# Kernel optimization log

Measured on AMD Instinct MI355X. Metric: run time of the kernel, lower is better.

The kernel has to match this reference:

```python
import jax, jax.numpy as jnp
import numpy as np

TIME_STEP = 3  # init_kwargs time_step
D = 512       # input_dim
N = 1024      # node_num
B = 16        # batch


def setup_inputs() -> dict:
    key = jax.random.key(0)
    ks = jax.random.split(key, 16)
    x = jax.random.normal(ks[0], (B, N, D), dtype=jnp.float32)
    # adjacency in [0,1), scaled by 1/N so repeated propagation stays well-conditioned
    in_matrix = jax.random.uniform(ks[1], (N, N), dtype=jnp.float32) / N
    out_matrix = jax.random.uniform(ks[2], (N, N), dtype=jnp.float32) / N
    s = 0.02
    w3w = jax.random.normal(ks[3], (D, 2 * D), dtype=jnp.float32) * s
    b3w = jnp.zeros((D,), dtype=jnp.float32)
    w3u = jax.random.normal(ks[4], (D, D), dtype=jnp.float32) * s
    b3u = jnp.zeros((D,), dtype=jnp.float32)
    w4w = jax.random.normal(ks[5], (D, 2 * D), dtype=jnp.float32) * s
    b4w = jnp.zeros((D,), dtype=jnp.float32)
    w5w = jax.random.normal(ks[6], (D, 2 * D), dtype=jnp.float32) * s
    b5w = jnp.zeros((D,), dtype=jnp.float32)
    w5u = jax.random.normal(ks[7], (D, D), dtype=jnp.float32) * s
    b5u = jnp.zeros((D,), dtype=jnp.float32)
    return {"x": x, "in_matrix": in_matrix, "out_matrix": out_matrix,
            "w3w": w3w, "b3w": b3w, "w3u": w3u, "b3u": b3u,
            "w4w": w4w, "b4w": b4w, "w5w": w5w, "b5w": b5w,
            "w5u": w5u, "b5u": b5u}


def reference(x, in_matrix, out_matrix, w3w, b3w, w3u, b3u, w4w, b4w, w5w, b5w, w5u, b5u):
    # x: [B, N, D]; in/out_matrix: [N, N] (shared across batch, as in torch repeat)
    nodes = x
    for _ in range(TIME_STEP):
        a_in = jnp.einsum('mn,bnd->bmd', in_matrix, nodes)   # [B,N,D]
        a_out = jnp.einsum('mn,bnd->bmd', out_matrix, nodes)  # [B,N,D]
        av = jnp.concatenate([a_in, a_out], axis=-1)           # [B,N,2D]
        f = nodes
        u3 = jnp.einsum('bnd,ed->bne', f, w3u) + b3u           # shared eq3_u term
        zv = jax.nn.sigmoid(jnp.einsum('bnc,ec->bne', av, w3w) + b3w + u3)
        # NOTE: original code reuses fc_eq3_u inside rv (faithful reproduction)
        rv = jax.nn.sigmoid(jnp.einsum('bnc,ec->bne', av, w4w) + b4w + u3)
        hv = jnp.tanh(jnp.einsum('bnc,ec->bne', av, w5w) + b5w
                      + jnp.einsum('bnd,ed->bne', rv * f, w5u) + b5u)
        nodes = (1.0 - zv) * f + zv * hv  # dropout p=0 -> identity
    return (nodes, in_matrix)
```

## Files before the change

kernel.cpp:

```cpp
#include <hip/hip_runtime.h>
#include <cstdint>
#include <cstddef>


#define B_ 16
#define N_ 1024
#define D_ 512
#define S_ (B_ * N_)
#define TWO_D 1024

typedef __attribute__((ext_vector_type(8))) short short8;
typedef __attribute__((ext_vector_type(4))) short s16x4;
typedef __attribute__((ext_vector_type(4))) float f32x4;

#define EPI_AVU3 0
#define EPI_BIG  2
#define EPI_G4   3

__device__ __forceinline__ float bf2f(short u) {
  union { unsigned int i; float f; } v;
  v.i = ((unsigned int)(unsigned short)u) << 16;
  return v.f;
}
__device__ __forceinline__ short f2bf(float f) {
  union { float f; unsigned int i; } v;
  v.f = f;
  unsigned int x = v.i;
  unsigned int r = (x + 0x7fffu + ((x >> 16) & 1u)) >> 16;
  return (short)(unsigned short)r;
}
__device__ __forceinline__ float fast_sigmoid(float x) {
  return __builtin_amdgcn_rcpf(1.f + __expf(-x));
}
__device__ __forceinline__ float fast_tanh(float x) {
  const float t = __expf(-2.f * fabsf(x));
  const float th = (1.f - t) * __builtin_amdgcn_rcpf(1.f + t);
  return __builtin_copysignf(th, x);
}

__device__ __forceinline__ void gload16(const void* g, void* l) {
  __builtin_amdgcn_global_load_lds(
      (__attribute__((address_space(1))) void*)g,
      (__attribute__((address_space(3))) void*)l, 16, 0, 0);
}

template <int EPI>
__global__ __launch_bounds__(512, 4) void gemm_nt(
    const short* A, const short* A2, int lda,
    const short* Bw, const short* Bw2, const short* Bw3, int ldb, int Kin,
    const float* bias0, const float* bias1, const float* bias2,
    const short* u3, const short* fcur,
    const short* hvp, const short* zvp,
    short* out0, short* out1, short* out2,
    float* outf, int twoC) {
  __shared__ __align__(16) short lds_a[128 * 32];
  __shared__ __align__(16) short lds_b[128 * 32];

  const int tid = threadIdx.x;
  const int lane = tid & 63;
  const int wave = tid >> 6;
  const int wr = wave >> 2;
  const int wc = wave & 3;

  int bx = blockIdx.x, by = blockIdx.y, bz = blockIdx.z;
  if constexpr (EPI == EPI_AVU3) {
    const int total = gridDim.x * gridDim.y * gridDim.z;
    const int id = (bz * gridDim.y + by) * gridDim.x + bx;
    if ((total & 7) == 0) {
      const int a = id & 7, m = id >> 3;
      const int l = a * (total >> 3) + m;
      bx = l & 3;
      by = (l >> 2) & 7;
      bz = l >> 5;
    }
  } else {
    const int gx = gridDim.x, gy = gridDim.y;
    if ((gy & 7) == 0) {
      const int id = by * gx + bx;
      const int a = id & 7;
      const int m = id >> 3;
      const int per = gy >> 3;
      by = a * per + m / gx;
      bx = m % gx;
    }
  }

  int m0 = by * 128;
  const int n0 = bx * 128;
  int K = Kin;

  const short* Aeff = A;
  const short* Beff = Bw;
  int lda_e = lda, ldb_e = ldb;
  int nb0 = n0;
  bool isU3 = false;
  int b_ = 0, j_ = 0;
  if constexpr (EPI == EPI_AVU3) {
    if (bz < twoC) {
      b_ = bz >> 1;
      j_ = bz & 1;
      Aeff = j_ ? A2 : A;
      Beff = Bw + (size_t)b_ * ((size_t)D_ * N_);
      lda_e = N_; ldb_e = N_; K = N_;
    } else {
      isU3 = true;
      const int b = bz - twoC;
      Aeff = u3  + (size_t)b * N_ * D_;
      Beff = Bw3 ;
      lda_e = D_; ldb_e = D_; K = D_;
      b_ = b;
    }
  } else if constexpr (EPI == EPI_BIG) {
    if (n0 < 512) { Beff = Bw; nb0 = n0; }
    else if (n0 < 1024) { Beff = Bw2; nb0 = n0 - 512; }
    else { Beff = Bw3; nb0 = n0 - 1024; }
  }

  f32x4 acc[4][2];
#pragma unroll
  for (int i = 0; i < 4; i++)
#pragma unroll
    for (int j = 0; j < 2; j++) acc[i][j] = (f32x4){0.f, 0.f, 0.f, 0.f};

  const int ar = tid >> 2;
  const int sc = tid & 3;
  const int qg = (sc - (ar >> 1)) & 3;
  const int ac = qg * 8;
  char* la = (char*)lds_a + tid * 16;
  char* lb = (char*)lds_b + tid * 16;
  const short* ga0 = Aeff + (size_t)(m0 + ar) * lda_e + ac;
  const short* gb0 = Beff + (size_t)(nb0 + ar) * ldb_e + ac;

  const int lm = lane & 15;
  const int qq = lane >> 4;

  int offA[4], offB[2];
#pragma unroll
  for (int i = 0; i < 4; i++) {
    const int Ra = wr * 64 + i * 16 + lm;
    offA[i] = Ra * 64 + (((qq + (Ra >> 1)) & 3) << 4);
  }
#pragma unroll
  for (int j = 0; j < 2; j++) {
    const int Rb = wc * 32 + j * 16 + lm;
    offB[j] = Rb * 64 + (((qq + (Rb >> 1)) & 3) << 4);
  }

  for (int k0 = 0; k0 < K; k0 += 32) {
    __syncthreads();
    gload16(ga0 + k0, la);
    gload16(gb0 + k0, lb);
    __syncthreads();

    short8 af[4], bfr[2];
#pragma unroll
    for (int i = 0; i < 4; i++)
      af[i] = *(const short8*)((const char*)lds_a + offA[i]);
#pragma unroll
    for (int j = 0; j < 2; j++)
      bfr[j] = *(const short8*)((const char*)lds_b + offB[j]);
#pragma unroll
    for (int i = 0; i < 4; i++)
#pragma unroll
      for (int j = 0; j < 2; j++)
        acc[i][j] = __builtin_amdgcn_mfma_f32_16x16x32_bf16(
            af[i], bfr[j], acc[i][j], 0, 0, 0);
  }

  const int r0 = (lane >> 4) * 4;
#pragma unroll
  for (int i = 0; i < 4; i++) {
#pragma unroll
    for (int j = 0; j < 2; j++) {
#pragma unroll
      for (int r = 0; r < 4; r++) {
        const int grow = m0 + wr * 64 + i * 16 + r0 + r;
        const int gcol = n0 + wc * 32 + j * 16 + lm;
        const float v = acc[i][j][r];
        if constexpr (EPI == EPI_AVU3) {
          if (!isU3) {
            out0[((size_t)(b_ * N_ + grow)) * TWO_D + j_ * D_ + gcol] =
                f2bf(v);
          } else {
            out1[((size_t)(b_ * N_ + grow)) * D_ + gcol] =
                f2bf(v + bias0[gcol]);
          }
        } else if constexpr (EPI == EPI_BIG) {
          if (gcol < 512) {
            const size_t sidx = (size_t)grow * D_ + gcol;
            const float x = v + bias0[gcol] + bf2f(u3[sidx]);
            out0[sidx] = f2bf(fast_sigmoid(x));
          } else if (gcol < 1024) {
            const int e = gcol - 512;
            const size_t sidx = (size_t)grow * D_ + e;
            const float x = v + bias1[e] + bf2f(u3[sidx]);
            out1[sidx] = f2bf(fast_sigmoid(x) * bf2f(fcur[sidx]));
          } else {
            const int e = gcol - 1024;
            const size_t sidx = (size_t)grow * D_ + e;
            out2[sidx] = f2bf(v + bias2[e]);
          }
        } else {
          const size_t sidx = (size_t)grow * D_ + gcol;
          const float x = bf2f(hvp[sidx]) + v + bias0[gcol];
          const float hv = fast_tanh(x);
          const float z = bf2f(zvp[sidx]);
          const float f = bf2f(fcur[sidx]);
          const float res = (1.f - z) * f + z * hv;
          if (outf) outf[sidx] = res;
          else out0[sidx] = f2bf(res);
        }
      }
    }
  }
}

__global__ void transpose_bnd(const short* __restrict__ in,
                              short* __restrict__ out) {
  __shared__ short tile[32][33];
  const int b = blockIdx.z;
  const int n0 = blockIdx.y * 32;
  const int d0 = blockIdx.x * 32;
  const int tx = threadIdx.x, ty = threadIdx.y;
  const short* ip = in + (size_t)b * N_ * D_;
  short* op = out + (size_t)b * N_ * D_;
#pragma unroll
  for (int yy = ty; yy < 32; yy += 8)
    tile[yy][tx] = ip[(size_t)(n0 + yy) * D_ + d0 + tx];
  __syncthreads();
#pragma unroll
  for (int yy = ty; yy < 32; yy += 8)
    op[(size_t)(d0 + yy) * N_ + n0 + tx] = tile[tx][yy];
}

struct CvtJobs {
  const float* src[8];
  short* dst[8];
  int end4[8];
  int tot4;
};
__global__ void cvt_all(CvtJobs j) {
  for (int idx = blockIdx.x * 256 + threadIdx.x; idx < j.tot4;
       idx += gridDim.x * 256) {
    int k = 0, start = 0;
#pragma unroll
    for (int t = 0; t < 8; t++) {
      if (idx >= j.end4[t]) { k = t + 1; start = j.end4[t]; }
    }
    const int rel = idx - start;
    const f32x4 v = ((const f32x4*)j.src[k])[rel];
    s16x4 o;
#pragma unroll
    for (int r = 0; r < 4; r++) o[r] = f2bf(v[r]);
    ((s16x4*)j.dst[k])[rel] = o;
  }
}

extern "C" void kernel_launch(void* const* d_in, const int* in_sizes, int n_in,
                              void* d_out, int out_size, void* d_ws,
                              size_t ws_size, hipStream_t stream) {
  const float* x = (const float*)d_in[0];
  const float* inM = (const float*)d_in[1];
  const float* outM = (const float*)d_in[2];
  const float* w3w = (const float*)d_in[3];
  const float* b3w = (const float*)d_in[4];
  const float* w3u = (const float*)d_in[5];
  const float* b3u = (const float*)d_in[6];
  const float* w4w = (const float*)d_in[7];
  const float* b4w = (const float*)d_in[8];
  const float* w5w = (const float*)d_in[9];
  const float* b5w = (const float*)d_in[10];
  const float* w5u = (const float*)d_in[11];
  const float* b5u = (const float*)d_in[12];
  float* outF = (float*)d_out;

  char* ws = (char*)d_ws;
  size_t off = 0;
  auto alloc = [&](size_t elems) {
    short* p = (short*)(ws + off);
    off = (off + elems * 2 + 255) & ~(size_t)255;
    return p;
  };
  short* nodes = alloc((size_t)S_ * D_);
  short* inMb = alloc((size_t)N_ * N_);
  short* outMb = alloc((size_t)N_ * N_);
  short* w3wb = alloc((size_t)512 * 1024);
  short* w4wb = alloc((size_t)512 * 1024);
  short* w5wb = alloc((size_t)512 * 1024);
  short* w3ub = alloc((size_t)D_ * D_);
  short* w5ub = alloc((size_t)D_ * D_);
  const size_t fixed = off;

  int C = 1;
  for (int c = 16; c >= 1; c >>= 1) {
    const size_t need = fixed + (size_t)7 * c * N_ * D_ * 2 + 8 * 256;
    if (need <= ws_size) { C = c; break; }
  }
  short* T = alloc((size_t)C * D_ * N_);
  short* av = alloc((size_t)C * N_ * TWO_D);
  short* u3 = alloc((size_t)C * N_ * D_);
  short* zv = alloc((size_t)C * N_ * D_);
  short* rf = alloc((size_t)C * N_ * D_);
  short* hvp = alloc((size_t)C * N_ * D_);

  CvtJobs cj;
  const int xs4 = S_ * D_ / 4, nn4 = N_ * N_ / 4;
  const int dd4 = D_ * D_ / 4, wd4 = 512 * 1024 / 4;
  const float* srcs[8] = {x, inM, outM, w3w, w4w, w5w, w3u, w5u};
  short* dsts[8] = {nodes, inMb, outMb, w3wb, w4wb, w5wb, w3ub, w5ub};
  const int lens[8] = {xs4, nn4, nn4, wd4, wd4, wd4, dd4, dd4};
  int cum = 0;
  for (int i = 0; i < 8; i++) {
    cj.src[i] = srcs[i];
    cj.dst[i] = dsts[i];
    cum += lens[i];
    cj.end4[i] = cum;
  }
  cj.tot4 = cum;
  cvt_all<<<1536, 256, 0, stream>>>(cj);
  hipMemcpyAsync(outF + (size_t)S_ * D_, inM, (size_t)N_ * N_ * 4,
                 hipMemcpyDeviceToDevice, stream);

  const dim3 tb32(32, 8);
  const dim3 tg(D_ / 32, N_ / 32, C);
  const dim3 g_avu3(D_ / 128, N_ / 128, 3 * C);
  const dim3 g_d(D_ / 128, C * N_ / 128, 1);
  const dim3 g_big(1536 / 128, C * N_ / 128, 1);

  const int nchunks = B_ / C;
  for (int c = 0; c < nchunks; ++c) {
    short* nodes_c = nodes + (size_t)c * C * N_ * D_;
    float* outF_c = outF + (size_t)c * C * N_ * D_;
    for (int step = 0; step < 3; ++step) {
      transpose_bnd<<<tg, tb32, 0, stream>>>(nodes_c, T);
      gemm_nt<EPI_AVU3><<<g_avu3, 512, 0, stream>>>(
          inMb, outMb, N_, T, nullptr, w3ub, N_, N_, b3u, nullptr, nullptr,
          nodes_c, nullptr, nullptr, nullptr, av, u3, nullptr, nullptr,
          2 * C);
      gemm_nt<EPI_BIG><<<g_big, 512, 0, stream>>>(
          av, nullptr, TWO_D, w3wb, w4wb, w5wb, TWO_D, TWO_D, b3w, b4w, b5w,
          u3, nodes_c, nullptr, nullptr, zv, rf, hvp, nullptr, 0);
      float* outf = (step == 2) ? outF_c : nullptr;
      gemm_nt<EPI_G4><<<g_d, 512, 0, stream>>>(
          rf, nullptr, D_, w5ub, nullptr, nullptr, D_, D_, b5u, nullptr,
          nullptr, nullptr, nodes_c, hvp, zv, nodes_c, nullptr, nullptr,
          outf, 0);
    }
  }
}
```

Baseline: 668.0 us.

## Double-buffer LDS tiles in GEMM to overlap global loads with MFMA

Adds a second pair of LDS buffers for the A and B tiles and restructures the K loop to prefetch the next 32-wide K slice while MFMAs consume the current one. This halves the number of barriers per K step and is meant to hide global-to-LDS load latency behind compute. LDS usage doubles to 32 KB per block, which may cut occupancy at 4 blocks of 512 threads per CU. The loop also assumes K is a multiple of 64.

New measurement: 636.8 us, median of 2. 1.05x faster.

```diff
diff --git a/kernel.cpp b/kernel.cpp
--- a/kernel.cpp
+++ b/kernel.cpp
@@ -53,8 +53,10 @@
     const short* hvp, const short* zvp,
     short* out0, short* out1, short* out2,
     float* outf, int twoC) {
-  __shared__ __align__(16) short lds_a[128 * 32];
-  __shared__ __align__(16) short lds_b[128 * 32];
+  __shared__ __align__(16) short lds_a0[128 * 32];
+  __shared__ __align__(16) short lds_b0[128 * 32];
+  __shared__ __align__(16) short lds_a1[128 * 32];
+  __shared__ __align__(16) short lds_b1[128 * 32];
 
   const int tid = threadIdx.x;
   const int lane = tid & 63;
@@ -126,8 +128,10 @@
   const int sc = tid & 3;
   const int qg = (sc - (ar >> 1)) & 3;
   const int ac = qg * 8;
-  char* la = (char*)lds_a + tid * 16;
-  char* lb = (char*)lds_b + tid * 16;
+  char* la0p = (char*)lds_a0 + tid * 16;
+  char* lb0p = (char*)lds_b0 + tid * 16;
+  char* la1p = (char*)lds_a1 + tid * 16;
+  char* lb1p = (char*)lds_b1 + tid * 16;
   const short* ga0 = Aeff + (size_t)(m0 + ar) * lda_e + ac;
   const short* gb0 = Beff + (size_t)(nb0 + ar) * ldb_e + ac;
 
@@ -146,26 +150,37 @@
     offB[j] = Rb * 64 + (((qq + (Rb >> 1)) & 3) << 4);
   }
 
-  for (int k0 = 0; k0 < K; k0 += 32) {
+#define COMPUTE_TILE(LA, LB)                                                 \
+  do {                                                                       \
+    short8 af[4], bfr[2];                                                    \
+    _Pragma("unroll") for (int i = 0; i < 4; i++)                            \
+        af[i] = *(const short8*)((const char*)(LA) + offA[i]);               \
+    _Pragma("unroll") for (int j = 0; j < 2; j++)                            \
+        bfr[j] = *(const short8*)((const char*)(LB) + offB[j]);              \
+    _Pragma("unroll") for (int i = 0; i < 4; i++)                            \
+        _Pragma("unroll") for (int j = 0; j < 2; j++)                        \
+            acc[i][j] = __builtin_amdgcn_mfma_f32_16x16x32_bf16(             \
+                af[i], bfr[j], acc[i][j], 0, 0, 0);                          \
+  } while (0)
+
+  gload16(ga0, la0p);
+  gload16(gb0, lb0p);
+  __syncthreads();
+
+  for (int k0 = 0; k0 < K; k0 += 64) {
+    gload16(ga0 + k0 + 32, la1p);
+    gload16(gb0 + k0 + 32, lb1p);
+    COMPUTE_TILE(lds_a0, lds_b0);
     __syncthreads();
-    gload16(ga0 + k0, la);
-    gload16(gb0 + k0, lb);
+
+    if (k0 + 64 < K) {
+      gload16(ga0 + k0 + 64, la0p);
+      gload16(gb0 + k0 + 64, lb0p);
+    }
+    COMPUTE_TILE(lds_a1, lds_b1);
     __syncthreads();
-
-    short8 af[4], bfr[2];
-#pragma unroll
-    for (int i = 0; i < 4; i++)
-      af[i] = *(const short8*)((const char*)lds_a + offA[i]);
-#pragma unroll
-    for (int j = 0; j < 2; j++)
-      bfr[j] = *(const short8*)((const char*)lds_b + offB[j]);
-#pragma unroll
-    for (int i = 0; i < 4; i++)
-#pragma unroll
-      for (int j = 0; j < 2; j++)
-        acc[i][j] = __builtin_amdgcn_mfma_f32_16x16x32_bf16(
-            af[i], bfr[j], acc[i][j], 0, 0, 0);
-  }
+  }
+#undef COMPUTE_TILE
 
   const int r0 = (lane >> 4) * 4;
 #pragma unroll
```

## Rewrite GEMM as 256x256 tiles with double-buffered LDS and ping-pong MFMA phases

Applied to the files above, without the earlier changes.

Replaces the 128x128, K=32, fully synchronized GEMM loop with a 256x256 tile over K=64 steps. Each operand is split into two 128-row halves held in double-buffered LDS, and async global-to-LDS loads for the next tile are issued between four MFMA phases. The code adds explicit vmcnt waits, sched barriers and setprio, and uses an XOR swizzle for the LDS layout. The goal is to hide load latency and raise arithmetic intensity per block. In exchange it uses far more LDS and registers (launch bounds lowered to 2), and the grids shrink, which may leave CUs underfilled at small batch chunks.

Result: slower. 911.1 us (+36.4%).

```diff
diff --git a/kernel.cpp b/kernel.cpp
--- a/kernel.cpp
+++ b/kernel.cpp
@@ -44,8 +44,16 @@
       (__attribute__((address_space(3))) void*)l, 16, 0, 0);
 }
 
+#define WAITV_IMM(N) asm volatile("s_waitcnt vmcnt(" #N ")" ::: "memory")
+#define WAITV(N) WAITV_IMM(N)
+#define LGKM0 asm volatile("s_waitcnt lgkmcnt(0)" ::: "memory")
+#define BAR() __builtin_amdgcn_s_barrier()
+#define SCHEDB() __builtin_amdgcn_sched_barrier(0)
+#define PRIO1 __builtin_amdgcn_s_setprio(1)
+#define PRIO0 __builtin_amdgcn_s_setprio(0)
+
 template <int EPI>
-__global__ __launch_bounds__(512, 4) void gemm_nt(
+__global__ __launch_bounds__(512, 2) void gemm_nt(
     const short* A, const short* A2, int lda,
     const short* Bw, const short* Bw2, const short* Bw3, int ldb, int Kin,
     const float* bias0, const float* bias1, const float* bias2,
@@ -53,14 +61,20 @@
     const short* hvp, const short* zvp,
     short* out0, short* out1, short* out2,
     float* outf, int twoC) {
-  __shared__ __align__(16) short lds_a[128 * 32];
-  __shared__ __align__(16) short lds_b[128 * 32];
+  __shared__ __align__(16) short sA00[8192];
+  __shared__ __align__(16) short sA01[8192];
+  __shared__ __align__(16) short sB00[8192];
+  __shared__ __align__(16) short sB01[8192];
+  __shared__ __align__(16) short sA10[8192];
+  __shared__ __align__(16) short sA11[8192];
+  __shared__ __align__(16) short sB10[8192];
+  __shared__ __align__(16) short sB11[8192];
 
   const int tid = threadIdx.x;
   const int lane = tid & 63;
   const int wave = tid >> 6;
-  const int wr = wave >> 2;
-  const int wc = wave & 3;
+  const int wm = wave & 3;
+  const int wn = wave >> 2;
 
   int bx = blockIdx.x, by = blockIdx.y, bz = blockIdx.z;
   if constexpr (EPI == EPI_AVU3) {
@@ -69,9 +83,9 @@
     if ((total & 7) == 0) {
       const int a = id & 7, m = id >> 3;
       const int l = a * (total >> 3) + m;
-      bx = l & 3;
-      by = (l >> 2) & 7;
-      bz = l >> 5;
+      bx = l & 1;
+      by = (l >> 1) & 3;
+      bz = l >> 3;
     }
   } else {
     const int gx = gridDim.x, gy = gridDim.y;
@@ -85,8 +99,8 @@
     }
   }
 
-  int m0 = by * 128;
-  const int n0 = bx * 128;
+  int m0 = by * 256;
+  const int n0 = bx * 256;
   int K = Kin;
 
   const short* Aeff = A;
@@ -116,99 +130,176 @@
     else { Beff = Bw3; nb0 = n0 - 1024; }
   }
 
-  f32x4 acc[4][2];
-#pragma unroll
-  for (int i = 0; i < 4; i++)
-#pragma unroll
-    for (int j = 0; j < 2; j++) acc[i][j] = (f32x4){0.f, 0.f, 0.f, 0.f};
-
-  const int ar = tid >> 2;
-  const int sc = tid & 3;
-  const int qg = (sc - (ar >> 1)) & 3;
-  const int ac = qg * 8;
-  char* la = (char*)lds_a + tid * 16;
-  char* lb = (char*)lds_b + tid * 16;
-  const short* ga0 = Aeff + (size_t)(m0 + ar) * lda_e + ac;
-  const short* gb0 = Beff + (size_t)(nb0 + ar) * ldb_e + ac;
+  f32x4 acc[2][2][2][4];
+#pragma unroll
+  for (int R = 0; R < 2; R++)
+#pragma unroll
+    for (int Cq = 0; Cq < 2; Cq++)
+#pragma unroll
+      for (int fm = 0; fm < 2; fm++)
+#pragma unroll
+        for (int fn = 0; fn < 4; fn++)
+          acc[R][Cq][fm][fn] = (f32x4){0.f, 0.f, 0.f, 0.f};
 
   const int lm = lane & 15;
   const int qq = lane >> 4;
-
-  int offA[4], offB[2];
-#pragma unroll
-  for (int i = 0; i < 4; i++) {
-    const int Ra = wr * 64 + i * 16 + lm;
-    offA[i] = Ra * 64 + (((qq + (Ra >> 1)) & 3) << 4);
-  }
-#pragma unroll
-  for (int j = 0; j < 2; j++) {
-    const int Rb = wc * 32 + j * 16 + lm;
-    offB[j] = Rb * 64 + (((qq + (Rb >> 1)) & 3) << 4);
-  }
-
-  for (int k0 = 0; k0 < K; k0 += 32) {
-    __syncthreads();
-    gload16(ga0 + k0, la);
-    gload16(gb0 + k0, lb);
-    __syncthreads();
-
-    short8 af[4], bfr[2];
-#pragma unroll
-    for (int i = 0; i < 4; i++)
-      af[i] = *(const short8*)((const char*)lds_a + offA[i]);
-#pragma unroll
-    for (int j = 0; j < 2; j++)
-      bfr[j] = *(const short8*)((const char*)lds_b + offB[j]);
-#pragma unroll
-    for (int i = 0; i < 4; i++)
-#pragma unroll
-      for (int j = 0; j < 2; j++)
-        acc[i][j] = __builtin_amdgcn_mfma_f32_16x16x32_bf16(
-            af[i], bfr[j], acc[i][j], 0, 0, 0);
-  }
-
-  const int r0 = (lane >> 4) * 4;
-#pragma unroll
-  for (int i = 0; i < 4; i++) {
-#pragma unroll
-    for (int j = 0; j < 2; j++) {
-#pragma unroll
-      for (int r = 0; r < 4; r++) {
-        const int grow = m0 + wr * 64 + i * 16 + r0 + r;
-        const int gcol = n0 + wc * 32 + j * 16 + lm;
-        const float v = acc[i][j][r];
-        if constexpr (EPI == EPI_AVU3) {
-          if (!isU3) {
-            out0[((size_t)(b_ * N_ + grow)) * TWO_D + j_ * D_ + gcol] =
-                f2bf(v);
-          } else {
-            out1[((size_t)(b_ * N_ + grow)) * D_ + gcol] =
-                f2bf(v + bias0[gcol]);
+  int offA[2][2], offB[4][2];
+#pragma unroll
+  for (int fm = 0; fm < 2; fm++)
+#pragma unroll
+    for (int ks = 0; ks < 2; ks++) {
+      const int rw = wm * 32 + fm * 16 + lm;
+      offA[fm][ks] = rw * 128 + (((ks * 4 + qq) ^ (lm & 7)) << 4);
+    }
+#pragma unroll
+  for (int fn = 0; fn < 4; fn++)
+#pragma unroll
+    for (int ks = 0; ks < 2; ks++) {
+      const int rw = wn * 64 + fn * 16 + lm;
+      offB[fn][ks] = rw * 128 + (((ks * 4 + qq) ^ (lm & 7)) << 4);
+    }
+
+  const int rr = tid >> 3;
+  const int qv = ((tid & 7) ^ (rr & 7)) * 8;
+  const short* pA00 = Aeff + (size_t)(m0 + rr) * lda_e + qv;
+  const short* pA01 = Aeff + (size_t)(m0 + 64 + rr) * lda_e + qv;
+  const short* pA10 = Aeff + (size_t)(m0 + 128 + rr) * lda_e + qv;
+  const short* pA11 = Aeff + (size_t)(m0 + 192 + rr) * lda_e + qv;
+  const short* pB00 = Beff + (size_t)(nb0 + rr) * ldb_e + qv;
+  const short* pB01 = Beff + (size_t)(nb0 + 64 + rr) * ldb_e + qv;
+  const short* pB10 = Beff + (size_t)(nb0 + 128 + rr) * ldb_e + qv;
+  const short* pB11 = Beff + (size_t)(nb0 + 192 + rr) * ldb_e + qv;
+  const int dst0 = tid * 16;
+  const int dst1 = 8192 + tid * 16;
+
+#define STAGE_A0(ARR, kn) do { \
+    gload16(pA00 + (size_t)(kn) * 64, (char*)ARR + dst0); \
+    gload16(pA01 + (size_t)(kn) * 64, (char*)ARR + dst1); } while (0)
+#define STAGE_A1(ARR, kn) do { \
+    gload16(pA10 + (size_t)(kn) * 64, (char*)ARR + dst0); \
+    gload16(pA11 + (size_t)(kn) * 64, (char*)ARR + dst1); } while (0)
+#define STAGE_B0(ARR, kn) do { \
+    gload16(pB00 + (size_t)(kn) * 64, (char*)ARR + dst0); \
+    gload16(pB01 + (size_t)(kn) * 64, (char*)ARR + dst1); } while (0)
+#define STAGE_B1(ARR, kn) do { \
+    gload16(pB10 + (size_t)(kn) * 64, (char*)ARR + dst0); \
+    gload16(pB11 + (size_t)(kn) * 64, (char*)ARR + dst1); } while (0)
+
+  short8 a0f[2][2], a1f[2][2], bfrag[4][2];
+
+#define READ_A(dst, ARR) \
+  _Pragma("unroll") for (int fm = 0; fm < 2; fm++) \
+  _Pragma("unroll") for (int ks = 0; ks < 2; ks++) \
+      dst[fm][ks] = *(const short8*)((const char*)ARR + offA[fm][ks]);
+#define READ_B(ARR) \
+  _Pragma("unroll") for (int fn = 0; fn < 4; fn++) \
+  _Pragma("unroll") for (int ks = 0; ks < 2; ks++) \
+      bfrag[fn][ks] = *(const short8*)((const char*)ARR + offB[fn][ks]);
+#define PHASE_MFMA(R, Cq, AF) \
+  _Pragma("unroll") for (int fm = 0; fm < 2; fm++) \
+  _Pragma("unroll") for (int fn = 0; fn < 4; fn++) \
+  _Pragma("unroll") for (int ks = 0; ks < 2; ks++) \
+      acc[R][Cq][fm][fn] = __builtin_amdgcn_mfma_f32_16x16x32_bf16( \
+          AF[fm][ks], bfrag[fn][ks], acc[R][Cq][fm][fn], 0, 0, 0);
+
+#define TILE_BODY(cA0_, cA1_, cB0_, cB1_, oA0_, oA1_, oB0_, oB1_, kn, DS, \
+                  G0_, G1_, G2_) \
+  do { \
+    WAITV(G0_); BAR(); SCHEDB(); \
+    READ_A(a0f, cA0_); READ_B(cB0_); \
+    if (DS) STAGE_A0(oA0_, kn); \
+    LGKM0; SCHEDB(); \
+    PRIO1; PHASE_MFMA(0, 0, a0f); PRIO0; \
+    WAITV(G1_); BAR(); SCHEDB(); \
+    READ_A(a1f, cA1_); \
+    if (DS) STAGE_B0(oB0_, kn); \
+    LGKM0; SCHEDB(); \
+    PRIO1; PHASE_MFMA(1, 0, a1f); PRIO0; \
+    WAITV(G2_); BAR(); SCHEDB(); \
+    READ_B(cB1_); \
+    if (DS) STAGE_A1(oA1_, kn); \
+    LGKM0; SCHEDB(); \
+    PRIO1; PHASE_MFMA(1, 1, a1f); PRIO0; \
+    if (DS) STAGE_B1(oB1_, kn); \
+    PRIO1; PHASE_MFMA(0, 1, a0f); PRIO0; \
+  } while (0)
+
+  const int KT = K >> 6;
+
+  STAGE_A0(sA00, 0);
+  STAGE_B0(sB00, 0);
+  STAGE_A1(sA01, 0);
+  STAGE_B1(sB01, 0);
+
+  int t = 0;
+  for (; t + 2 < KT; t += 2) {
+    TILE_BODY(sA00, sA01, sB00, sB01, sA10, sA11, sB10, sB11, t + 1, 1,
+              4, 4, 4);
+    TILE_BODY(sA10, sA11, sB10, sB11, sA00, sA01, sB00, sB01, t + 2, 1,
+              4, 4, 4);
+  }
+  TILE_BODY(sA00, sA01, sB00, sB01, sA10, sA11, sB10, sB11, KT - 1, 1,
+            4, 4, 4);
+  TILE_BODY(sA10, sA11, sB10, sB11, sA00, sA01, sB00, sB01, 0, 0,
+            4, 2, 0);
+
+#undef TILE_BODY
+#undef PHASE_MFMA
+#undef READ_A
+#undef READ_B
+#undef STAGE_A0
+#undef STAGE_A1
+#undef STAGE_B0
+#undef STAGE_B1
+
+  const int r4 = lane >> 4;
+#pragma unroll
+  for (int R = 0; R < 2; R++) {
+#pragma unroll
+    for (int Cq = 0; Cq < 2; Cq++) {
+#pragma unroll
+      for (int fm = 0; fm < 2; fm++) {
+#pragma unroll
+        for (int fn = 0; fn < 4; fn++) {
+#pragma unroll
+          for (int r = 0; r < 4; r++) {
+            const int grow = m0 + R * 128 + wm * 32 + fm * 16 + r4 * 4 + r;
+            const int gcol = n0 + Cq * 128 + wn * 64 + fn * 16 + lm;
+            const float v = acc[R][Cq][fm][fn][r];
+            if constexpr (EPI == EPI_AVU3) {
+              if (!isU3) {
+                out0[((size_t)(b_ * N_ + grow)) * TWO_D + j_ * D_ + gcol] =
+                    f2bf(v);
+              } else {
+                out1[((size_t)(b_ * N_ + grow)) * D_ + gcol] =
+                    f2bf(v + bias0[gcol]);
+              }
+            } else if constexpr (EPI == EPI_BIG) {
+              if (gcol < 512) {
+                const size_t sidx = (size_t)grow * D_ + gcol;
+                const float x = v + bias0[gcol] + bf2f(u3[sidx]);
+                out0[sidx] = f2bf(fast_sigmoid(x));
+              } else if (gcol < 1024) {
+                const int e = gcol - 512;
+                const size_t sidx = (size_t)grow * D_ + e;
+                const float x = v + bias1[e] + bf2f(u3[sidx]);
+                out1[sidx] = f2bf(fast_sigmoid(x) * bf2f(fcur[sidx]));
+              } else {
+                const int e = gcol - 1024;
+                const size_t sidx = (size_t)grow * D_ + e;
+                out2[sidx] = f2bf(v + bias2[e]);
+              }
+            } else {
+              const size_t sidx = (size_t)grow * D_ + gcol;
+              const float x = bf2f(hvp[sidx]) + v + bias0[gcol];
+              const float hv = fast_tanh(x);
+              const float z = bf2f(zvp[sidx]);
+              const float f = bf2f(fcur[sidx]);
+              const float res = (1.f - z) * f + z * hv;
+              if (outf) outf[sidx] = res;
+              else out0[sidx] = f2bf(res);
+            }
           }
-        } else if constexpr (EPI == EPI_BIG) {
-          if (gcol < 512) {
-            const size_t sidx = (size_t)grow * D_ + gcol;
-            const float x = v + bias0[gcol] + bf2f(u3[sidx]);
-            out0[sidx] = f2bf(fast_sigmoid(x));
-          } else if (gcol < 1024) {
-            const int e = gcol - 512;
-            const size_t sidx = (size_t)grow * D_ + e;
-            const float x = v + bias1[e] + bf2f(u3[sidx]);
-            out1[sidx] = f2bf(fast_sigmoid(x) * bf2f(fcur[sidx]));
-          } else {
-            const int e = gcol - 1024;
-            const size_t sidx = (size_t)grow * D_ + e;
-            out2[sidx] = f2bf(v + bias2[e]);
-          }
-        } else {
-          const size_t sidx = (size_t)grow * D_ + gcol;
-          const float x = bf2f(hvp[sidx]) + v + bias0[gcol];
-          const float hv = fast_tanh(x);
-          const float z = bf2f(zvp[sidx]);
-          const float f = bf2f(fcur[sidx]);
-          const float res = (1.f - z) * f + z * hv;
-          if (outf) outf[sidx] = res;
-          else out0[sidx] = f2bf(res);
         }
       }
     }
@@ -323,9 +414,9 @@
 
   const dim3 tb32(32, 8);
   const dim3 tg(D_ / 32, N_ / 32, C);
-  const dim3 g_avu3(D_ / 128, N_ / 128, 3 * C);
-  const dim3 g_d(D_ / 128, C * N_ / 128, 1);
-  const dim3 g_big(1536 / 128, C * N_ / 128, 1);
+  const dim3 g_avu3(D_ / 256, N_ / 256, 3 * C);
+  const dim3 g_d(D_ / 256, C * N_ / 256, 1);
+  const dim3 g_big(1536 / 256, C * N_ / 256, 1);
 
   const int nchunks = B_ / C;
   for (int c = 0; c < nchunks; ++c) {
```
